# Kernel optimization log

Hardware: AMD Instinct MI355X
Metric: run time of the kernel (lower is better)

The kernel has to match this reference:

```python
import jax, jax.numpy as jnp
import numpy as np

TOP_K = 2
ALPHA = 1.702
LIMIT = 7.0


def setup_inputs() -> dict:
    key = jax.random.key(0)
    ks = jax.random.split(key, 7)
    B, S, H, I, E = 1, 2048, 1024, 1024, 8
    scale = 0.02
    return {
        "hidden_states": jax.random.normal(ks[0], (B, S, H), dtype=jnp.float32),
        "router_w": jax.random.normal(ks[1], (H, E), dtype=jnp.float32) * scale,
        "router_b": jax.random.normal(ks[2], (E,), dtype=jnp.float32) * scale,
        "gate_up_proj": jax.random.normal(ks[3], (E, H, 2 * I), dtype=jnp.float32) * scale,
        "gate_up_bias": jax.random.normal(ks[4], (E, 2 * I), dtype=jnp.float32) * scale,
        "down_proj": jax.random.normal(ks[5], (E, I, H), dtype=jnp.float32) * scale,
        "down_bias": jax.random.normal(ks[6], (E, H), dtype=jnp.float32) * scale,
    }


def reference(hidden_states, router_w, router_b, gate_up_proj, gate_up_bias, down_proj, down_bias):
    # hidden_states: [B, S, H]; gate_up_proj: [E, H, 2I]; down_proj: [E, I, H]
    E = gate_up_proj.shape[0]
    # --- router (GPT-OSS style): top-k logits, softmax over top-k, scatter to E slots ---
    logits = jnp.einsum("bsh,he->bse", hidden_states, router_w) + router_b  # [B,S,E]
    top_vals, top_idx = jax.lax.top_k(logits, TOP_K)                         # [B,S,K]
    topk_weights = jax.nn.softmax(top_vals, axis=-1)                         # [B,S,K]
    onehot = jax.nn.one_hot(top_idx, E, dtype=logits.dtype)                  # [B,S,K,E]
    router_scores = jnp.einsum("bsk,bske->bse", topk_weights, onehot)        # [B,S,E]
    # --- expert compute (dense over the small expert axis; selection via gather below,
    #     which matches the sparsity-masked grouped matmul + all_to_all_combine math) ---
    gu = jnp.einsum("bsh,ehf->bsef", hidden_states, gate_up_proj) + gate_up_bias  # [B,S,E,2I]
    gate = gu[..., 0::2]  # interleaved gate
    up = gu[..., 1::2]    # interleaved up
    gate = jnp.minimum(gate, LIMIT)
    up = jnp.maximum(jnp.minimum(up, LIMIT), -LIMIT)
    glu = gate * jax.nn.sigmoid(gate * ALPHA)
    activated = (up + 1.0) * glu                                             # [B,S,E,I]
    down = jnp.einsum("bsei,eih->bseh", activated, down_proj) + down_bias    # [B,S,E,H]
    # combine: gather each token's K selected expert outputs, weighted sum
    sel = jnp.take_along_axis(down, top_idx[..., None], axis=2)              # [B,S,K,H]
    output = jnp.einsum("bskh,bsk->bsh", sel, topk_weights)                  # [B,S,H]
    return output, router_scores
```

## Files before the change

### kernel.cpp

```cpp
#include <hip/hip_runtime.h>
#include <stdint.h>


#define Sd 2048
#define Hd 1024
#define Id 1024

typedef __bf16 bf16x8 __attribute__((ext_vector_type(8)));
typedef _Float16 f16x8 __attribute__((ext_vector_type(8)));
typedef float f32x4 __attribute__((ext_vector_type(4)));

__device__ __forceinline__ f32x4 mfma_bf16(bf16x8 a, bf16x8 b, f32x4 c) {
  return __builtin_amdgcn_mfma_f32_16x16x32_bf16(a, b, c, 0, 0, 0);
}

__device__ __forceinline__ void gload16(const __bf16* g, __bf16* l) {
  __builtin_amdgcn_global_load_lds(
      (const __attribute__((address_space(1))) unsigned int*)g,
      (__attribute__((address_space(3))) unsigned int*)l, 16, 0, 0);
}

__device__ __forceinline__ unsigned int packbf(float lo, float hi) {
  __bf16 a = (__bf16)lo, b = (__bf16)hi;
  return (unsigned int)__builtin_bit_cast(unsigned short, a) |
         ((unsigned int)__builtin_bit_cast(unsigned short, b) << 16);
}

__global__ __launch_bounds__(256) void k_router(
    const float* __restrict__ x, const float* __restrict__ rw,
    const float* __restrict__ rb, float* __restrict__ scores,
    float* __restrict__ topw, int* __restrict__ eid,
    __bf16* __restrict__ xb) {
  const int lane = threadIdx.x & 63;
  const int t = blockIdx.x * 4 + (threadIdx.x >> 6);
  float acc[8];
#pragma unroll
  for (int e = 0; e < 8; ++e) acc[e] = 0.f;
  const float* xr = x + (size_t)t * Hd;
  unsigned int* xbo = (unsigned int*)(xb + (size_t)t * Hd);
#pragma unroll
  for (int j = 0; j < 8; ++j) {
    int h = j * 128 + lane * 2;
    float2 xv = *(const float2*)(xr + h);
    xbo[h >> 1] = packbf(xv.x, xv.y);
    const float4* wp = (const float4*)(rw + h * 8);
    float4 a0 = wp[0], a1 = wp[1], b0 = wp[2], b1 = wp[3];
    acc[0] += xv.x * a0.x; acc[1] += xv.x * a0.y;
    acc[2] += xv.x * a0.z; acc[3] += xv.x * a0.w;
    acc[4] += xv.x * a1.x; acc[5] += xv.x * a1.y;
    acc[6] += xv.x * a1.z; acc[7] += xv.x * a1.w;
    acc[0] += xv.y * b0.x; acc[1] += xv.y * b0.y;
    acc[2] += xv.y * b0.z; acc[3] += xv.y * b0.w;
    acc[4] += xv.y * b1.x; acc[5] += xv.y * b1.y;
    acc[6] += xv.y * b1.z; acc[7] += xv.y * b1.w;
  }
#pragma unroll
  for (int m = 32; m >= 1; m >>= 1) {
#pragma unroll
    for (int e = 0; e < 8; ++e) acc[e] += __shfl_xor(acc[e], m, 64);
  }
  if (lane == 0) {
    float lg[8];
#pragma unroll
    for (int e = 0; e < 8; ++e) lg[e] = acc[e] + rb[e];
    int i0 = 0; float v0 = lg[0];
#pragma unroll
    for (int e = 1; e < 8; ++e) if (lg[e] > v0) { v0 = lg[e]; i0 = e; }
    int i1 = -1; float v1 = -3.4e38f;
#pragma unroll
    for (int e = 0; e < 8; ++e) if (e != i0 && lg[e] > v1) { v1 = lg[e]; i1 = e; }
    float e1 = __expf(v1 - v0);
    float s = 1.f + e1;
    float w0 = 1.f / s, w1v = e1 / s;
#pragma unroll
    for (int e = 0; e < 8; ++e)
      scores[t * 8 + e] = (e == i0) ? w0 : ((e == i1) ? w1v : 0.f);
    topw[t * 2] = w0;
    topw[t * 2 + 1] = w1v;
    eid[t] = i0 | (i1 << 4);
  }
}

__global__ __launch_bounds__(256) void k_assign(
    const int* __restrict__ eid, int* __restrict__ cnt,
    int* __restrict__ assign, int* __restrict__ tokmap) {
  __shared__ int lcnt[8];
  const int tid = threadIdx.x;
  if (tid < 8) lcnt[tid] = 0;
  __syncthreads();
  for (int t = tid; t < 2048; t += 256) {
    int v = eid[t];
    int i0 = v & 15, i1 = v >> 4;
    int s0 = atomicAdd(&lcnt[i0], 1);
    assign[i0 * 2048 + s0] = t * 2;
    tokmap[t * 2] = (i0 << 11) | s0;
    int s1 = atomicAdd(&lcnt[i1], 1);
    assign[i1 * 2048 + s1] = t * 2 + 1;
    tokmap[t * 2 + 1] = (i1 << 11) | s1;
  }
  __syncthreads();
  if (tid < 8) cnt[tid] = lcnt[tid];
}

__global__ __launch_bounds__(256) void k_gather(
    const __bf16* __restrict__ xb, const int* __restrict__ cnt,
    const int* __restrict__ assign, __bf16* __restrict__ xg) {
  const int u = blockIdx.x;
  int acc = 0, myE = -1, myU0 = 0, nE = 0;
#pragma unroll
  for (int q = 0; q < 8; ++q) {
    int units = ((cnt[q] + 255) >> 8) * 16;
    if (u >= acc && u < acc + units) { myE = q; myU0 = acc; nE = cnt[q]; }
    acc += units;
  }
  if (myE < 0) return;
  const int lane = threadIdx.x & 63;
  const int wv = threadIdx.x >> 6;
  const int row = lane & 15, koff = (lane >> 4) * 8;
  const int slot = (u - myU0) * 16 + row;
  const bool valid = slot < nE;
  int tok = 0;
  if (valid) tok = assign[myE * 2048 + slot] >> 1;
  const __bf16* src = xb + (size_t)tok * Hd + koff;
#pragma unroll
  for (int s = 0; s < 8; ++s) {
    int k32 = wv + 4 * s;
    bf16x8 v;
#pragma unroll
    for (int j = 0; j < 8; ++j) v[j] = (__bf16)0.f;
    if (valid) v = *(const bf16x8*)(src + k32 * 32);
    *(bf16x8*)(xg + (((size_t)u * 32 + k32) * 64 + lane) * 8) = v;
  }
}

__global__ __launch_bounds__(256) void k_pre1(const float* __restrict__ wgu,
                                              __bf16* __restrict__ w1f) {
  const int b = blockIdx.x;
  const int nt = b & 7, kt = (b >> 3) & 15, e = b >> 7;
  __shared__ unsigned int Ls[16][16][34];
  const int tid = threadIdx.x;
  const int w = tid >> 6, lane = tid & 63;
  const float* src = wgu + (size_t)e * (1024 * 2048) +
                     (size_t)(kt * 64 + w * 16) * 2048 + nt * 256;
  const int i0 = lane * 2;
  const int c0 = i0 & 15, u0 = (i0 >> 4) * 2;
  const int c1 = (i0 + 1) & 15, u1 = ((i0 + 1) >> 4) * 2;
#pragma unroll
  for (int rp = 0; rp < 8; ++rp) {
    float4 fa = *(const float4*)(src + (size_t)(rp * 2) * 2048 + lane * 4);
    float4 fb = *(const float4*)(src + (size_t)(rp * 2 + 1) * 2048 + lane * 4);
    int r = w * 8 + rp;
    Ls[u0][c0][r] = packbf(fa.x, fb.x);
    Ls[u0 + 1][c0][r] = packbf(fa.y, fb.y);
    Ls[u1][c1][r] = packbf(fa.z, fb.z);
    Ls[u1 + 1][c1][r] = packbf(fa.w, fb.w);
  }
  __syncthreads();
  const int khi = lane >> 4, c = lane & 15;
#pragma unroll
  for (int uu = 0; uu < 8; ++uu) {
    int ul = w * 8 + uu, vu = ul >> 1, k32l = ul & 1;
    const unsigned int* p = &Ls[vu][c][k32l * 16 + khi * 4];
    uint2 q0 = *(const uint2*)p;
    uint2 q1 = *(const uint2*)(p + 2);
    int itg = nt * 8 + (vu >> 1), vf = vu & 1;
    size_t row = ((size_t)(e * 64 + itg) * 2 + vf) * 32 + (kt * 2 + k32l);
    uint4 o = {q0.x, q0.y, q1.x, q1.y};
    *(uint4*)(w1f + row * 512 + lane * 8) = o;
  }
}

__global__ __launch_bounds__(256) void k_pre2(const float* __restrict__ wdn,
                                              __bf16* __restrict__ w2f) {
  const int b = blockIdx.x;
  const int nt = b & 3, kt = (b >> 2) & 15, e = b >> 6;
  __shared__ unsigned int Ls[16][16][34];
  const int tid = threadIdx.x;
  const int w = tid >> 6, lane = tid & 63;
  const float* src = wdn + (size_t)e * (1024 * 1024) +
                     (size_t)(kt * 64 + w * 16) * 1024 + nt * 256;
#pragma unroll
  for (int rp = 0; rp < 8; ++rp) {
    float4 fa = *(const float4*)(src + (size_t)(rp * 2) * 1024 + lane * 4);
    float4 fb = *(const float4*)(src + (size_t)(rp * 2 + 1) * 1024 + lane * 4);
    int r = w * 8 + rp;
    float va[4] = {fa.x, fa.y, fa.z, fa.w};
    float vb[4] = {fb.x, fb.y, fb.z, fb.w};
#pragma unroll
    for (int q = 0; q < 4; ++q) {
      int cl = lane * 4 + q;
      Ls[cl >> 4][cl & 15][r] = packbf(va[q], vb[q]);
    }
  }
  __syncthreads();
  const int khi = lane >> 4, c = lane & 15;
#pragma unroll
  for (int uu = 0; uu < 8; ++uu) {
    int ul = w * 8 + uu, Fl = ul >> 1, k32l = ul & 1;
    const unsigned int* p = &Ls[Fl][c][k32l * 16 + khi * 4];
    uint2 q0 = *(const uint2*)p;
    uint2 q1 = *(const uint2*)(p + 2);
    size_t row = (size_t)(e * 64 + nt * 16 + Fl) * 32 + (kt * 2 + k32l);
    uint4 o = {q0.x, q0.y, q1.x, q1.y};
    *(uint4*)(w2f + row * 512 + lane * 8) = o;
  }
}

__global__ __launch_bounds__(512, 4) void k_gemm1(
    const __bf16* __restrict__ xg, const __bf16* __restrict__ w1f,
    const float* __restrict__ gub, const int* __restrict__ cnt,
    __bf16* __restrict__ abuf) {
  const int e = blockIdx.x & 7;
  const int it = blockIdx.x >> 3;
  const int n = cnt[e];
  if (n <= 0) return;
  __shared__ __align__(16) __bf16 Bs[2][32][512];
  __shared__ __align__(16) __bf16 Ts[256][16];
  const int tid = threadIdx.x;
  const int lane = tid & 63;
  const int wv = tid >> 6;

  const __bf16* wbase = w1f + (size_t)((e * 64 + it) * 2) * (32 * 512);
  __bf16* bsf = &Bs[0][0][0];
#pragma unroll
  for (int s = 0; s < 8; ++s) {
    int idx = s * 512 + tid;
    gload16(wbase + (size_t)idx * 8, bsf + (size_t)idx * 8);
  }
  const int iCol = it * 16 + (lane & 15);
  const float bg = gub[e * 2048 + 2 * iCol];
  const float bu = gub[e * 2048 + 2 * iCol + 1];
  int eb = 0;
#pragma unroll
  for (int q = 0; q < 8; ++q) eb += (q < e) ? (((cnt[q] + 255) >> 8) << 8) : 0;
  const int u0 = eb >> 4;
  const int nmt = (n + 255) >> 8;

  for (int mt = 0; mt < nmt; ++mt) {
    __syncthreads();
    const __bf16* ap0 =
        xg + ((size_t)(u0 + mt * 16 + 2 * wv) * 32) * 512 + lane * 8;
    const __bf16* ap1 = ap0 + (size_t)32 * 512;
    f32x4 acc[2][2];
#pragma unroll
    for (int a = 0; a < 2; ++a)
#pragma unroll
      for (int b = 0; b < 2; ++b) acc[a][b] = (f32x4){0.f, 0.f, 0.f, 0.f};
    bf16x8 pf[8][2];
#pragma unroll
    for (int d = 0; d < 8; ++d) {
      pf[d][0] = *(const bf16x8*)(ap0 + d * 512);
      pf[d][1] = *(const bf16x8*)(ap1 + d * 512);
    }
#pragma unroll 8
    for (int ks = 0; ks < 24; ++ks) {
      bf16x8 b0 = *(const bf16x8*)&Bs[0][ks][lane * 8];
      bf16x8 b1 = *(const bf16x8*)&Bs[1][ks][lane * 8];
      acc[0][0] = mfma_bf16(pf[ks & 7][0], b0, acc[0][0]);
      acc[0][1] = mfma_bf16(pf[ks & 7][0], b1, acc[0][1]);
      acc[1][0] = mfma_bf16(pf[ks & 7][1], b0, acc[1][0]);
      acc[1][1] = mfma_bf16(pf[ks & 7][1], b1, acc[1][1]);
      pf[ks & 7][0] = *(const bf16x8*)(ap0 + (ks + 8) * 512);
      pf[ks & 7][1] = *(const bf16x8*)(ap1 + (ks + 8) * 512);
    }
#pragma unroll
    for (int ks = 24; ks < 32; ++ks) {
      bf16x8 b0 = *(const bf16x8*)&Bs[0][ks][lane * 8];
      bf16x8 b1 = *(const bf16x8*)&Bs[1][ks][lane * 8];
      acc[0][0] = mfma_bf16(pf[ks & 7][0], b0, acc[0][0]);
      acc[0][1] = mfma_bf16(pf[ks & 7][0], b1, acc[0][1]);
      acc[1][0] = mfma_bf16(pf[ks & 7][1], b0, acc[1][0]);
      acc[1][1] = mfma_bf16(pf[ks & 7][1], b1, acc[1][1]);
    }
#pragma unroll
    for (int mi = 0; mi < 2; ++mi) {
#pragma unroll
      for (int rr = 0; rr < 4; ++rr) {
        int row = wv * 32 + mi * 16 + (lane >> 4) * 4 + rr;
        float g = fminf(acc[mi][0][rr] + bg, 7.f);
        float u = fminf(fmaxf(acc[mi][1][rr] + bu, -7.f), 7.f);
        float sg = 1.f / (1.f + __expf(-1.702f * g));
        Ts[row][lane & 15] = (__bf16)((u + 1.f) * (g * sg));
      }
    }
    __syncthreads();
    {
      int r = tid & 15, hl = (tid >> 4) & 1, sbl = tid >> 5;
      bf16x8 v = *(const bf16x8*)&Ts[sbl * 16 + r][hl * 8];
      size_t o = (((size_t)(u0 + mt * 16 + sbl) * 32) + (it >> 1)) * 512 +
                 ((((it & 1) * 2 + hl) * 16 + r) * 8);
      *(bf16x8*)(abuf + o) = v;
    }
  }
}

__global__ __launch_bounds__(512, 4) void k_gemm2(
    const __bf16* __restrict__ abuf, const __bf16* __restrict__ w2f,
    const float* __restrict__ dnb, const int* __restrict__ cnt,
    const int* __restrict__ assign, const float* __restrict__ topw,
    _Float16* __restrict__ dbuf) {
  const int e = blockIdx.x & 7;
  const int rdec = blockIdx.x >> 3;
  const int ms = rdec & 1;
  const int ht = rdec >> 1;
  const int n = cnt[e];
  if (n <= 0) return;
  __shared__ __align__(16) __bf16 Bs[2][32][512];
  __shared__ float wgt[256];
  const int tid = threadIdx.x;
  const int lane = tid & 63;
  const int wv = tid >> 6;

  const __bf16* wbase = w2f + (size_t)(e * 64 + ht * 2) * (32 * 512);
  __bf16* bsf = &Bs[0][0][0];
#pragma unroll
  for (int s = 0; s < 8; ++s) {
    int idx = s * 512 + tid;
    gload16(wbase + (size_t)idx * 8, bsf + (size_t)idx * 8);
  }
  int eb = 0;
#pragma unroll
  for (int q = 0; q < 8; ++q) eb += (q < e) ? (((cnt[q] + 255) >> 8) << 8) : 0;
  const int u0 = eb >> 4;
  const int nmt = (n + 255) >> 8;

  for (int mt = ms; mt < nmt; mt += 2) {
    __syncthreads();
    if (tid < 256) {
      int slot = mt * 256 + tid;
      int en = (slot < n) ? assign[e * 2048 + slot] : -1;
      wgt[tid] = (en >= 0) ? topw[en] : 0.f;
    }
    __syncthreads();
    const __bf16* ab0 =
        abuf + ((size_t)(u0 + mt * 16 + 2 * wv) * 32) * 512 + lane * 8;
    const __bf16* ab1 = ab0 + (size_t)32 * 512;
    f32x4 acc[2][2];
#pragma unroll
    for (int a = 0; a < 2; ++a)
#pragma unroll
      for (int b = 0; b < 2; ++b) acc[a][b] = (f32x4){0.f, 0.f, 0.f, 0.f};
    bf16x8 pf[8][2];
#pragma unroll
    for (int d = 0; d < 8; ++d) {
      pf[d][0] = *(const bf16x8*)(ab0 + d * 512);
      pf[d][1] = *(const bf16x8*)(ab1 + d * 512);
    }
#pragma unroll 8
    for (int ks = 0; ks < 24; ++ks) {
      bf16x8 b0 = *(const bf16x8*)&Bs[0][ks][lane * 8];
      bf16x8 b1 = *(const bf16x8*)&Bs[1][ks][lane * 8];
      acc[0][0] = mfma_bf16(pf[ks & 7][0], b0, acc[0][0]);
      acc[0][1] = mfma_bf16(pf[ks & 7][0], b1, acc[0][1]);
      acc[1][0] = mfma_bf16(pf[ks & 7][1], b0, acc[1][0]);
      acc[1][1] = mfma_bf16(pf[ks & 7][1], b1, acc[1][1]);
      pf[ks & 7][0] = *(const bf16x8*)(ab0 + (ks + 8) * 512);
      pf[ks & 7][1] = *(const bf16x8*)(ab1 + (ks + 8) * 512);
    }
#pragma unroll
    for (int ks = 24; ks < 32; ++ks) {
      bf16x8 b0 = *(const bf16x8*)&Bs[0][ks][lane * 8];
      bf16x8 b1 = *(const bf16x8*)&Bs[1][ks][lane * 8];
      acc[0][0] = mfma_bf16(pf[ks & 7][0], b0, acc[0][0]);
      acc[0][1] = mfma_bf16(pf[ks & 7][0], b1, acc[0][1]);
      acc[1][0] = mfma_bf16(pf[ks & 7][1], b0, acc[1][0]);
      acc[1][1] = mfma_bf16(pf[ks & 7][1], b1, acc[1][1]);
    }
#pragma unroll
    for (int ni = 0; ni < 2; ++ni) {
      const int nn = ht * 32 + ni * 16 + (lane & 15);
      const float bias = dnb[e * 1024 + nn];
#pragma unroll
      for (int mi = 0; mi < 2; ++mi) {
#pragma unroll
        for (int rr = 0; rr < 4; ++rr) {
          int row = wv * 32 + mi * 16 + (lane >> 4) * 4 + rr;
          int slot = eb + mt * 256 + row;
          dbuf[(size_t)slot * 1024 + nn] =
              (_Float16)(wgt[row] * (acc[mi][ni][rr] + bias));
        }
      }
    }
  }
}

__global__ __launch_bounds__(256) void k_combine(
    const _Float16* __restrict__ dbuf, const int* __restrict__ tokmap,
    const int* __restrict__ cnt, float* __restrict__ out) {
  const int t = blockIdx.x * 4 + (threadIdx.x >> 6);
  const int lane = threadIdx.x & 63;
  int v0 = tokmap[t * 2], v1 = tokmap[t * 2 + 1];
  int e0 = v0 >> 11, e1 = v1 >> 11;
  int b0 = 0, b1 = 0, acc = 0;
#pragma unroll
  for (int q = 0; q < 8; ++q) {
    if (q == e0) b0 = acc;
    if (q == e1) b1 = acc;
    acc += ((cnt[q] + 255) >> 8) << 8;
  }
  const _Float16* r0 = dbuf + (size_t)(b0 + (v0 & 2047)) * 1024 + lane * 16;
  const _Float16* r1 = dbuf + (size_t)(b1 + (v1 & 2047)) * 1024 + lane * 16;
  float* o = out + (size_t)t * 1024 + lane * 16;
#pragma unroll
  for (int h = 0; h < 2; ++h) {
    f16x8 a = *(const f16x8*)(r0 + h * 8);
    f16x8 b = *(const f16x8*)(r1 + h * 8);
    float4 o0, o1;
    o0.x = (float)a[0] + (float)b[0];
    o0.y = (float)a[1] + (float)b[1];
    o0.z = (float)a[2] + (float)b[2];
    o0.w = (float)a[3] + (float)b[3];
    o1.x = (float)a[4] + (float)b[4];
    o1.y = (float)a[5] + (float)b[5];
    o1.z = (float)a[6] + (float)b[6];
    o1.w = (float)a[7] + (float)b[7];
    *(float4*)(o + h * 8) = o0;
    *(float4*)(o + h * 8 + 4) = o1;
  }
}

extern "C" void kernel_launch(void* const* d_in, const int* in_sizes, int n_in,
                              void* d_out, int out_size, void* d_ws, size_t ws_size,
                              hipStream_t stream) {
  const float* x   = (const float*)d_in[0];
  const float* rw  = (const float*)d_in[1];
  const float* rb  = (const float*)d_in[2];
  const float* wgu = (const float*)d_in[3];
  const float* gub = (const float*)d_in[4];
  const float* wdn = (const float*)d_in[5];
  const float* dnb = (const float*)d_in[6];
  float* out = (float*)d_out;
  float* scores = out + (size_t)Sd * Hd;

  char* ws = (char*)d_ws;
  int* cnt     = (int*)ws;
  int* assign  = (int*)(ws + 256);
  float* topw  = (float*)(ws + 256 + 65536);
  int* tokmap  = (int*)(ws + 256 + 65536 + 16384);
  int* eid     = (int*)(ws + 256 + 65536 + 32768);
  __bf16* xg   = (__bf16*)(ws + ((size_t)1 << 20));
  __bf16* abuf = (__bf16*)(ws + ((size_t)15 << 20));
  __bf16* xb   = (__bf16*)(ws + ((size_t)28 << 20));
  __bf16* w1f  = (__bf16*)(ws + ((size_t)28 << 20));
  __bf16* w2f  = (__bf16*)(ws + ((size_t)28 << 20));
  _Float16* dbuf = (_Float16*)(ws + ((size_t)44 << 20));

  k_router<<<512, 256, 0, stream>>>(x, rw, rb, scores, topw, eid, xb);
  k_assign<<<1, 256, 0, stream>>>(eid, cnt, assign, tokmap);
  k_gather<<<384, 256, 0, stream>>>(xb, cnt, assign, xg);
  k_pre1<<<1024, 256, 0, stream>>>(wgu, w1f);
  k_gemm1<<<512, 512, 0, stream>>>(xg, w1f, gub, cnt, abuf);
  k_pre2<<<512, 256, 0, stream>>>(wdn, w2f);
  k_gemm2<<<512, 512, 0, stream>>>(abuf, w2f, dnb, cnt, assign, topw, dbuf);
  k_combine<<<512, 256, 0, stream>>>(dbuf, tokmap, cnt, out);
}
```

Measured before the change: 118.9 us.

## Retile expert GEMMs into 64x128 block tiles with per-k LDS staging

Both expert GEMM kernels move from a 256-row M tile with a fully LDS-resident 32-column weight slab to a 64x128 block tile staged one k-slice at a time through LDS. Four waves split the tile 2x2, each holding a 2x4 accumulator grid. The aim is more blocks, more parallelism, and more reuse of each weight slice across rows. In exchange, the loop now takes two barriers per k step and has no software prefetch or double buffering, so global load latency is exposed every iteration.

Result: slower. 141.9 us (+19.4%).

```diff
diff --git a/kernel.cpp b/kernel.cpp
--- a/kernel.cpp
+++ b/kernel.cpp
@@ -206,176 +206,178 @@
   }
 }
 
-__global__ __launch_bounds__(512, 4) void k_gemm1(
+__global__ __launch_bounds__(256) void k_gemm1(
     const __bf16* __restrict__ xg, const __bf16* __restrict__ w1f,
     const float* __restrict__ gub, const int* __restrict__ cnt,
     __bf16* __restrict__ abuf) {
   const int e = blockIdx.x & 7;
-  const int it = blockIdx.x >> 3;
+  const int r = blockIdx.x >> 3;
+  const int it = r & 15;
+  const int ms = r >> 4;
   const int n = cnt[e];
   if (n <= 0) return;
-  __shared__ __align__(16) __bf16 Bs[2][32][512];
-  __shared__ __align__(16) __bf16 Ts[256][16];
+  __shared__ __align__(16) __bf16 As[4][512];
+  __shared__ __align__(16) __bf16 Bs[8][512];
+  __shared__ __align__(16) __bf16 Ts[64][72];
   const int tid = threadIdx.x;
   const int lane = tid & 63;
-  const int wv = tid >> 6;
-
-  const __bf16* wbase = w1f + (size_t)((e * 64 + it) * 2) * (32 * 512);
-  __bf16* bsf = &Bs[0][0][0];
-#pragma unroll
-  for (int s = 0; s < 8; ++s) {
-    int idx = s * 512 + tid;
-    gload16(wbase + (size_t)idx * 8, bsf + (size_t)idx * 8);
-  }
-  const int iCol = it * 16 + (lane & 15);
-  const float bg = gub[e * 2048 + 2 * iCol];
-  const float bu = gub[e * 2048 + 2 * iCol + 1];
+  const int wid = tid >> 6;
+  const int wm = wid >> 1, wn = wid & 1;
+
+  const float bg = gub[e * 2048 + 2 * (it * 64 + (wn * 2 + 0) * 16 + (lane & 15))];
+  const float bu = gub[e * 2048 + 2 * (it * 64 + (wn * 2 + 0) * 16 + (lane & 15)) + 1];
+  const float bg1 = gub[e * 2048 + 2 * (it * 64 + (wn * 2 + 1) * 16 + (lane & 15))];
+  const float bu1 = gub[e * 2048 + 2 * (it * 64 + (wn * 2 + 1) * 16 + (lane & 15)) + 1];
   int eb = 0;
 #pragma unroll
   for (int q = 0; q < 8; ++q) eb += (q < e) ? (((cnt[q] + 255) >> 8) << 8) : 0;
   const int u0 = eb >> 4;
-  const int nmt = (n + 255) >> 8;
-
-  for (int mt = 0; mt < nmt; ++mt) {
+  const int eu = ((n + 255) >> 8) << 4;
+  const int nmt = eu >> 2;
+
+  for (int mt = ms; mt < nmt; mt += 8) {
+    f32x4 acc[2][4];
+#pragma unroll
+    for (int a = 0; a < 2; ++a)
+#pragma unroll
+      for (int b = 0; b < 4; ++b) acc[a][b] = (f32x4){0.f, 0.f, 0.f, 0.f};
+    for (int ks = 0; ks < 32; ++ks) {
+      __syncthreads();
+#pragma unroll
+      for (int s = 0; s < 3; ++s) {
+        int c = wid * 3 + s;
+        if (c < 4) {
+          gload16(xg + ((size_t)(u0 + mt * 4 + c) * 32 + ks) * 512 + lane * 8,
+                  &As[c][lane * 8]);
+        } else {
+          int v = c - 4;
+          int itg = it * 4 + (v >> 1), vf = v & 1;
+          gload16(w1f + ((size_t)((e * 64 + itg) * 2 + vf) * 32 + ks) * 512 +
+                      lane * 8,
+                  &Bs[v][lane * 8]);
+        }
+      }
+      __syncthreads();
+      bf16x8 a0 = *(const bf16x8*)&As[wm * 2 + 0][lane * 8];
+      bf16x8 a1 = *(const bf16x8*)&As[wm * 2 + 1][lane * 8];
+      bf16x8 b[4];
+#pragma unroll
+      for (int ni = 0; ni < 4; ++ni)
+        b[ni] = *(const bf16x8*)&Bs[wn * 4 + ni][lane * 8];
+#pragma unroll
+      for (int ni = 0; ni < 4; ++ni) {
+        acc[0][ni] = mfma_bf16(a0, b[ni], acc[0][ni]);
+        acc[1][ni] = mfma_bf16(a1, b[ni], acc[1][ni]);
+      }
+    }
+#pragma unroll
+    for (int p = 0; p < 2; ++p) {
+      const int colL = (wn * 2 + p) * 16 + (lane & 15);
+      const float bgp = p ? bg1 : bg;
+      const float bup = p ? bu1 : bu;
+#pragma unroll
+      for (int mi = 0; mi < 2; ++mi) {
+        f32x4 ag = acc[mi][2 * p];
+        f32x4 au = acc[mi][2 * p + 1];
+#pragma unroll
+        for (int rr = 0; rr < 4; ++rr) {
+          int row = wm * 32 + mi * 16 + (lane >> 4) * 4 + rr;
+          float g = fminf(ag[rr] + bgp, 7.f);
+          float u = fminf(fmaxf(au[rr] + bup, -7.f), 7.f);
+          float sg = 1.f / (1.f + __expf(-1.702f * g));
+          Ts[row][colL] = (__bf16)((u + 1.f) * (g * sg));
+        }
+      }
+    }
     __syncthreads();
-    const __bf16* ap0 =
-        xg + ((size_t)(u0 + mt * 16 + 2 * wv) * 32) * 512 + lane * 8;
-    const __bf16* ap1 = ap0 + (size_t)32 * 512;
-    f32x4 acc[2][2];
-#pragma unroll
-    for (int a = 0; a < 2; ++a)
-#pragma unroll
-      for (int b = 0; b < 2; ++b) acc[a][b] = (f32x4){0.f, 0.f, 0.f, 0.f};
-    bf16x8 pf[8][2];
-#pragma unroll
-    for (int d = 0; d < 8; ++d) {
-      pf[d][0] = *(const bf16x8*)(ap0 + d * 512);
-      pf[d][1] = *(const bf16x8*)(ap1 + d * 512);
-    }
-#pragma unroll 8
-    for (int ks = 0; ks < 24; ++ks) {
-      bf16x8 b0 = *(const bf16x8*)&Bs[0][ks][lane * 8];
-      bf16x8 b1 = *(const bf16x8*)&Bs[1][ks][lane * 8];
-      acc[0][0] = mfma_bf16(pf[ks & 7][0], b0, acc[0][0]);
-      acc[0][1] = mfma_bf16(pf[ks & 7][0], b1, acc[0][1]);
-      acc[1][0] = mfma_bf16(pf[ks & 7][1], b0, acc[1][0]);
-      acc[1][1] = mfma_bf16(pf[ks & 7][1], b1, acc[1][1]);
-      pf[ks & 7][0] = *(const bf16x8*)(ap0 + (ks + 8) * 512);
-      pf[ks & 7][1] = *(const bf16x8*)(ap1 + (ks + 8) * 512);
-    }
-#pragma unroll
-    for (int ks = 24; ks < 32; ++ks) {
-      bf16x8 b0 = *(const bf16x8*)&Bs[0][ks][lane * 8];
-      bf16x8 b1 = *(const bf16x8*)&Bs[1][ks][lane * 8];
-      acc[0][0] = mfma_bf16(pf[ks & 7][0], b0, acc[0][0]);
-      acc[0][1] = mfma_bf16(pf[ks & 7][0], b1, acc[0][1]);
-      acc[1][0] = mfma_bf16(pf[ks & 7][1], b0, acc[1][0]);
-      acc[1][1] = mfma_bf16(pf[ks & 7][1], b1, acc[1][1]);
-    }
-#pragma unroll
-    for (int mi = 0; mi < 2; ++mi) {
-#pragma unroll
-      for (int rr = 0; rr < 4; ++rr) {
-        int row = wv * 32 + mi * 16 + (lane >> 4) * 4 + rr;
-        float g = fminf(acc[mi][0][rr] + bg, 7.f);
-        float u = fminf(fmaxf(acc[mi][1][rr] + bu, -7.f), 7.f);
-        float sg = 1.f / (1.f + __expf(-1.702f * g));
-        Ts[row][lane & 15] = (__bf16)((u + 1.f) * (g * sg));
-      }
-    }
-    __syncthreads();
-    {
-      int r = tid & 15, hl = (tid >> 4) & 1, sbl = tid >> 5;
-      bf16x8 v = *(const bf16x8*)&Ts[sbl * 16 + r][hl * 8];
-      size_t o = (((size_t)(u0 + mt * 16 + sbl) * 32) + (it >> 1)) * 512 +
-                 ((((it & 1) * 2 + hl) * 16 + r) * 8);
+#pragma unroll
+    for (int h2 = 0; h2 < 2; ++h2) {
+      int idx = h2 * 256 + tid;
+      int l = idx & 63, u2 = idx >> 6;
+      int sbl = u2 >> 1, k32l = u2 & 1;
+      bf16x8 v = *(const bf16x8*)&Ts[sbl * 16 + (l & 15)][k32l * 32 + ((l >> 4) * 8)];
+      size_t o = ((size_t)(u0 + mt * 4 + sbl) * 32 + (it * 2 + k32l)) * 512 + l * 8;
       *(bf16x8*)(abuf + o) = v;
     }
   }
 }
 
-__global__ __launch_bounds__(512, 4) void k_gemm2(
+__global__ __launch_bounds__(256) void k_gemm2(
     const __bf16* __restrict__ abuf, const __bf16* __restrict__ w2f,
     const float* __restrict__ dnb, const int* __restrict__ cnt,
     const int* __restrict__ assign, const float* __restrict__ topw,
     _Float16* __restrict__ dbuf) {
   const int e = blockIdx.x & 7;
-  const int rdec = blockIdx.x >> 3;
-  const int ms = rdec & 1;
-  const int ht = rdec >> 1;
+  const int r = blockIdx.x >> 3;
+  const int ht = r & 7;
+  const int ms = r >> 3;
   const int n = cnt[e];
   if (n <= 0) return;
-  __shared__ __align__(16) __bf16 Bs[2][32][512];
-  __shared__ float wgt[256];
+  __shared__ __align__(16) __bf16 As[4][512];
+  __shared__ __align__(16) __bf16 Bs[8][512];
+  __shared__ float wgt[64];
   const int tid = threadIdx.x;
   const int lane = tid & 63;
-  const int wv = tid >> 6;
-
-  const __bf16* wbase = w2f + (size_t)(e * 64 + ht * 2) * (32 * 512);
-  __bf16* bsf = &Bs[0][0][0];
-#pragma unroll
-  for (int s = 0; s < 8; ++s) {
-    int idx = s * 512 + tid;
-    gload16(wbase + (size_t)idx * 8, bsf + (size_t)idx * 8);
-  }
+  const int wid = tid >> 6;
+  const int wm = wid >> 1, wn = wid & 1;
+
   int eb = 0;
 #pragma unroll
   for (int q = 0; q < 8; ++q) eb += (q < e) ? (((cnt[q] + 255) >> 8) << 8) : 0;
   const int u0 = eb >> 4;
-  const int nmt = (n + 255) >> 8;
-
-  for (int mt = ms; mt < nmt; mt += 2) {
+  const int eu = ((n + 255) >> 8) << 4;
+  const int nmt = eu >> 2;
+
+  for (int mt = ms; mt < nmt; mt += 8) {
     __syncthreads();
-    if (tid < 256) {
-      int slot = mt * 256 + tid;
+    if (tid < 64) {
+      int slot = mt * 64 + tid;
       int en = (slot < n) ? assign[e * 2048 + slot] : -1;
       wgt[tid] = (en >= 0) ? topw[en] : 0.f;
     }
-    __syncthreads();
-    const __bf16* ab0 =
-        abuf + ((size_t)(u0 + mt * 16 + 2 * wv) * 32) * 512 + lane * 8;
-    const __bf16* ab1 = ab0 + (size_t)32 * 512;
-    f32x4 acc[2][2];
+    f32x4 acc[2][4];
 #pragma unroll
     for (int a = 0; a < 2; ++a)
 #pragma unroll
-      for (int b = 0; b < 2; ++b) acc[a][b] = (f32x4){0.f, 0.f, 0.f, 0.f};
-    bf16x8 pf[8][2];
-#pragma unroll
-    for (int d = 0; d < 8; ++d) {
-      pf[d][0] = *(const bf16x8*)(ab0 + d * 512);
-      pf[d][1] = *(const bf16x8*)(ab1 + d * 512);
-    }
-#pragma unroll 8
-    for (int ks = 0; ks < 24; ++ks) {
-      bf16x8 b0 = *(const bf16x8*)&Bs[0][ks][lane * 8];
-      bf16x8 b1 = *(const bf16x8*)&Bs[1][ks][lane * 8];
-      acc[0][0] = mfma_bf16(pf[ks & 7][0], b0, acc[0][0]);
-      acc[0][1] = mfma_bf16(pf[ks & 7][0], b1, acc[0][1]);
-      acc[1][0] = mfma_bf16(pf[ks & 7][1], b0, acc[1][0]);
-      acc[1][1] = mfma_bf16(pf[ks & 7][1], b1, acc[1][1]);
-      pf[ks & 7][0] = *(const bf16x8*)(ab0 + (ks + 8) * 512);
-      pf[ks & 7][1] = *(const bf16x8*)(ab1 + (ks + 8) * 512);
-    }
-#pragma unroll
-    for (int ks = 24; ks < 32; ++ks) {
-      bf16x8 b0 = *(const bf16x8*)&Bs[0][ks][lane * 8];
-      bf16x8 b1 = *(const bf16x8*)&Bs[1][ks][lane * 8];
-      acc[0][0] = mfma_bf16(pf[ks & 7][0], b0, acc[0][0]);
-      acc[0][1] = mfma_bf16(pf[ks & 7][0], b1, acc[0][1]);
-      acc[1][0] = mfma_bf16(pf[ks & 7][1], b0, acc[1][0]);
-      acc[1][1] = mfma_bf16(pf[ks & 7][1], b1, acc[1][1]);
-    }
-#pragma unroll
-    for (int ni = 0; ni < 2; ++ni) {
-      const int nn = ht * 32 + ni * 16 + (lane & 15);
+      for (int b = 0; b < 4; ++b) acc[a][b] = (f32x4){0.f, 0.f, 0.f, 0.f};
+    for (int ks = 0; ks < 32; ++ks) {
+      __syncthreads();
+#pragma unroll
+      for (int s = 0; s < 3; ++s) {
+        int c = wid * 3 + s;
+        if (c < 4) {
+          gload16(abuf + ((size_t)(u0 + mt * 4 + c) * 32 + ks) * 512 + lane * 8,
+                  &As[c][lane * 8]);
+        } else {
+          int v = c - 4;
+          gload16(w2f + ((size_t)(e * 64 + ht * 8 + v) * 32 + ks) * 512 +
+                      lane * 8,
+                  &Bs[v][lane * 8]);
+        }
+      }
+      __syncthreads();
+      bf16x8 a0 = *(const bf16x8*)&As[wm * 2 + 0][lane * 8];
+      bf16x8 a1 = *(const bf16x8*)&As[wm * 2 + 1][lane * 8];
+      bf16x8 b[4];
+#pragma unroll
+      for (int ni = 0; ni < 4; ++ni)
+        b[ni] = *(const bf16x8*)&Bs[wn * 4 + ni][lane * 8];
+#pragma unroll
+      for (int ni = 0; ni < 4; ++ni) {
+        acc[0][ni] = mfma_bf16(a0, b[ni], acc[0][ni]);
+        acc[1][ni] = mfma_bf16(a1, b[ni], acc[1][ni]);
+      }
+    }
+#pragma unroll
+    for (int ni = 0; ni < 4; ++ni) {
+      const int nn = ht * 128 + (wn * 4 + ni) * 16 + (lane & 15);
       const float bias = dnb[e * 1024 + nn];
 #pragma unroll
       for (int mi = 0; mi < 2; ++mi) {
 #pragma unroll
         for (int rr = 0; rr < 4; ++rr) {
-          int row = wv * 32 + mi * 16 + (lane >> 4) * 4 + rr;
-          int slot = eb + mt * 256 + row;
+          int row = wm * 32 + mi * 16 + (lane >> 4) * 4 + rr;
+          int slot = eb + mt * 64 + row;
           dbuf[(size_t)slot * 1024 + nn] =
               (_Float16)(wgt[row] * (acc[mi][ni][rr] + bias));
         }
@@ -449,8 +451,8 @@
   k_assign<<<1, 256, 0, stream>>>(eid, cnt, assign, tokmap);
   k_gather<<<384, 256, 0, stream>>>(xb, cnt, assign, xg);
   k_pre1<<<1024, 256, 0, stream>>>(wgu, w1f);
-  k_gemm1<<<512, 512, 0, stream>>>(xg, w1f, gub, cnt, abuf);
+  k_gemm1<<<1024, 256, 0, stream>>>(xg, w1f, gub, cnt, abuf);
   k_pre2<<<512, 256, 0, stream>>>(wdn, w2f);
-  k_gemm2<<<512, 512, 0, stream>>>(abuf, w2f, dnb, cnt, assign, topw, dbuf);
+  k_gemm2<<<512, 256, 0, stream>>>(abuf, w2f, dnb, cnt, assign, topw, dbuf);
   k_combine<<<512, 256, 0, stream>>>(dbuf, tokmap, cnt, out);
 }
```
